# Optimization experiments

Measured on AMD Instinct MI355X. Metric: run time of the kernel, lower is better.

The kernel has to match this reference:

```python
import jax, jax.numpy as jnp
import numpy as np

N = 100000
E = 3200000
NODE_IN = 118
D = 32
H = 4
C = D // H  # 8
EDGE_DIM = 50 + 3
L = 4
LN_EPS = 1e-5


def _layernorm(x, g, b):
    mu = jnp.mean(x, axis=-1, keepdims=True)
    var = jnp.mean(jnp.square(x - mu), axis=-1, keepdims=True)
    return (x - mu) * jax.lax.rsqrt(var + LN_EPS) * g + b


def setup_inputs() -> dict:
    key = jax.random.key(0)
    ks = jax.random.split(key, 20)
    x = jax.random.normal(ks[0], (N, NODE_IN), dtype=jnp.float32)
    edge_index = jax.random.randint(ks[1], (2, E), 0, N, dtype=jnp.int32)
    edge_len = jax.random.normal(ks[2], (E, 50), dtype=jnp.float32)
    edge_vec = jax.random.normal(ks[3], (E, 3), dtype=jnp.float32)
    s_in = 1.0 / np.sqrt(NODE_IN)
    s_d = 1.0 / np.sqrt(D)
    s_e = 1.0 / np.sqrt(EDGE_DIM)
    node_in_W = jax.random.normal(ks[4], (NODE_IN, D), dtype=jnp.float32) * s_in
    node_in_b = jnp.zeros((D,), dtype=jnp.float32)
    ln_g = jnp.ones((L, D), dtype=jnp.float32)
    ln_b = jnp.zeros((L, D), dtype=jnp.float32)
    Wq = jax.random.normal(ks[5], (L, D, D), dtype=jnp.float32) * s_d
    bq = jnp.zeros((L, D), dtype=jnp.float32)
    Wk = jax.random.normal(ks[6], (L, D, D), dtype=jnp.float32) * s_d
    bk = jnp.zeros((L, D), dtype=jnp.float32)
    Wv = jax.random.normal(ks[7], (L, D, D), dtype=jnp.float32) * s_d
    bv = jnp.zeros((L, D), dtype=jnp.float32)
    We = jax.random.normal(ks[8], (L, EDGE_DIM, D), dtype=jnp.float32) * s_e  # lin_edge, bias=False
    Wskip = jax.random.normal(ks[9], (L, D, D), dtype=jnp.float32) * s_d
    bskip = jnp.zeros((L, D), dtype=jnp.float32)
    return {"x": x, "edge_index": edge_index, "edge_len": edge_len, "edge_vec": edge_vec,
            "node_in_W": node_in_W, "node_in_b": node_in_b, "ln_g": ln_g, "ln_b": ln_b,
            "Wq": Wq, "bq": bq, "Wk": Wk, "bk": bk, "Wv": Wv, "bv": bv,
            "We": We, "Wskip": Wskip, "bskip": bskip}


def reference(x, edge_index, edge_len, edge_vec, node_in_W, node_in_b, ln_g, ln_b,
              Wq, bq, Wk, bk, Wv, bv, We, Wskip, bskip):
    src = edge_index[0]  # j (source), messages flow source -> target
    dst = edge_index[1]  # i (target), softmax grouped by dst
    ef = jnp.concatenate([edge_len, edge_vec], axis=-1)  # [E, 53]
    h = x @ node_in_W + node_in_b  # [N, D]
    scale = 1.0 / np.sqrt(C)
    for l in range(L):
        xn = _layernorm(h, ln_g[l], ln_b[l])
        q = (xn @ Wq[l] + bq[l]).reshape(N, H, C)
        k = (xn @ Wk[l] + bk[l]).reshape(N, H, C)
        v = (xn @ Wv[l] + bv[l]).reshape(N, H, C)
        e = (ef @ We[l]).reshape(E, H, C)  # per-edge key/value shift
        kj = k[src] + e                     # [E, H, C]
        alpha = jnp.sum(q[dst] * kj, axis=-1) * scale  # [E, H]
        # segment softmax over incoming edges of each target node
        amax = jax.ops.segment_max(alpha, dst, num_segments=N)  # [N, H]
        amax = jnp.where(jnp.isfinite(amax), amax, 0.0)
        ex = jnp.exp(alpha - amax[dst])
        denom = jax.ops.segment_sum(ex, dst, num_segments=N)
        w = ex / (denom[dst] + 1e-16)       # [E, H]
        msg = (v[src] + e) * w[:, :, None]  # [E, H, C]
        agg = jax.ops.segment_sum(msg.reshape(E, H * C), dst, num_segments=N)  # [N, D]
        y = agg + xn @ Wskip[l] + bskip[l]  # concat heads + root skip (lin_skip(x_i))
        h = h + y                            # residual
    return h
```

## Files before the change

### kernel.cpp

```cpp
#include <hip/hip_runtime.h>
#include <hip/hip_bf16.h>
#include <math.h>

#define N_NODES 100000
#define N_EDGES 3200000
#define NODE_IN 118
#define DIM 32
#define EDF 53
#define NLAYER 4

typedef __attribute__((ext_vector_type(8))) short short8;
typedef __attribute__((ext_vector_type(4))) float f32x4;
typedef unsigned short u16;
typedef unsigned int u32;

static __device__ __forceinline__ float bfhi2f(u32 hi) {
    union { u32 i; float f; } x; x.i = hi; return x.f;
}
static __device__ __forceinline__ u16 f2bf(float f) {
    union { float f; u32 i; } x; x.f = f;
    u32 i = x.i;
    return (u16)((i + 0x7FFFu + ((i >> 16) & 1u)) >> 16);
}
static __device__ __forceinline__ u32 pk2bf(float a, float b) {
    u32 r;
    asm("v_cvt_pk_bf16_f32 %0, %1, %2" : "=v"(r) : "v"(a), "v"(b));
    return r;
}

__global__ __launch_bounds__(256) void k_count(const int* __restrict__ dst, int* __restrict__ cnt) {
    int e = blockIdx.x * 256 + threadIdx.x;
    atomicAdd(&cnt[dst[e]], 1);
}

__global__ __launch_bounds__(256) void k_scanA(const int* __restrict__ cnt, int* __restrict__ off,
                                               int* __restrict__ bsum) {
    __shared__ int s[256];
    int t = threadIdx.x; int i = blockIdx.x * 256 + t;
    int v = (i < N_NODES) ? cnt[i] : 0;
    s[t] = v; __syncthreads();
    for (int d = 1; d < 256; d <<= 1) {
        int x = (t >= d) ? s[t - d] : 0; __syncthreads();
        s[t] += x; __syncthreads();
    }
    if (i < N_NODES) off[i] = s[t] - v;
    if (t == 255) bsum[blockIdx.x] = s[t];
}

__global__ __launch_bounds__(512) void k_scanB(int* bsum, int nb) {
    __shared__ int s[512];
    int t = threadIdx.x;
    int v = (t < nb) ? bsum[t] : 0;
    s[t] = v; __syncthreads();
    for (int d = 1; d < 512; d <<= 1) {
        int x = (t >= d) ? s[t - d] : 0; __syncthreads();
        s[t] += x; __syncthreads();
    }
    if (t < nb) bsum[t] = s[t] - v;
}

__global__ __launch_bounds__(256) void k_scanC(int* off, const int* __restrict__ bsum) {
    int i = blockIdx.x * 256 + threadIdx.x;
    if (i < N_NODES) off[i] += bsum[blockIdx.x];
    if (i == 0) off[N_NODES] = N_EDGES;
}

__global__ __launch_bounds__(256) void k_fill(const int* __restrict__ src, const int* __restrict__ dst,
                                              const int* __restrict__ off, int* __restrict__ cur,
                                              int* __restrict__ eidx, int* __restrict__ esrc) {
    int e = blockIdx.x * 256 + threadIdx.x;
    int d = dst[e];
    int p = off[d] + atomicAdd(&cur[d], 1);
    eidx[p] = e;
    esrc[p] = src[e];
}

__global__ __launch_bounds__(256) void k_init(const float* __restrict__ x, const float* __restrict__ W,
                                              const float* __restrict__ b, float* __restrict__ h) {
    __shared__ float Ws[NODE_IN * DIM];
    __shared__ float xs[8][NODE_IN];
    int t = threadIdx.x;
    for (int i = t; i < NODE_IN * DIM; i += 256) Ws[i] = W[i];
    int nb = blockIdx.x * 8;
    for (int i = t; i < 8 * NODE_IN; i += 256) {
        int n = i / NODE_IN, j = i % NODE_IN;
        xs[n][j] = x[(size_t)(nb + n) * NODE_IN + j];
    }
    __syncthreads();
    int n = t >> 5, c = t & 31;
    float acc = b[c];
    #pragma unroll 2
    for (int j = 0; j < NODE_IN; j++) acc += xs[n][j] * Ws[j * DIM + c];
    h[(size_t)(nb + n) * DIM + c] = acc;
}

template <int NL>
__global__ __launch_bounds__(256) void k_egemm(const float* __restrict__ elen, const float* __restrict__ evec,
                                               const int* __restrict__ eidx, const float* __restrict__ We,
                                               u16* __restrict__ eout) {
    __shared__ u16 st[4][16 * 160];
    int tid = threadIdx.x;
    int lane = tid & 63;
    int wvl = tid >> 6;
    int wv = (blockIdx.x * 256 + tid) >> 6;
    int nw = (gridDim.x * 256) >> 6;
    int n15 = lane & 15, kb = lane >> 4;

    short8 bf[2][2 * NL];
    for (int s = 0; s < 2; s++) {
        for (int t = 0; t < 2 * NL; t++) {
            int n = t * 16 + n15;
            int lay = n >> 5, c = n & 31;
            short8 tmp;
            #pragma unroll
            for (int j = 0; j < 8; j++) {
                int kk = s * 32 + kb * 8 + j;
                float w = (kk < EDF) ? We[(size_t)lay * EDF * DIM + (size_t)kk * DIM + c] : 0.f;
                ((u16*)&tmp)[j] = f2bf(w);
            }
            bf[s][t] = tmp;
        }
    }

    const int NT = N_EDGES / 16;

    auto LOADD = [&](int eid, float* fv) {
        const float* lp = elen + (size_t)eid * 50;
        {
            const float2* p2 = (const float2*)(lp + kb * 8);
            #pragma unroll
            for (int j = 0; j < 4; j++) { float2 t2 = p2[j]; fv[2 * j] = t2.x; fv[2 * j + 1] = t2.y; }
        }
        if (kb < 2) {
            const float2* p2 = (const float2*)(lp + 32 + kb * 8);
            #pragma unroll
            for (int j = 0; j < 4; j++) { float2 t2 = p2[j]; fv[8 + 2 * j] = t2.x; fv[8 + 2 * j + 1] = t2.y; }
        } else if (kb == 2) {
            float2 t2 = *(const float2*)(lp + 48);
            const float* vp = evec + (size_t)eid * 3;
            fv[8] = t2.x; fv[9] = t2.y; fv[10] = vp[0]; fv[11] = vp[1]; fv[12] = vp[2];
            fv[13] = 0.f; fv[14] = 0.f; fv[15] = 0.f;
        } else {
            #pragma unroll
            for (int j = 8; j < 16; j++) fv[j] = 0.f;
        }
    };

    int eidA = (wv < NT) ? eidx[wv * 16 + n15] : 0;
    int t1 = wv + nw;
    int eidB = (t1 < NT) ? eidx[t1 * 16 + n15] : 0;
    float cur[16];
    if (wv < NT) LOADD(eidA, cur);

    for (int tile = wv; tile < NT; tile += nw) {
        int nxt = tile + nw;
        float nx[16];
        if (nxt < NT) LOADD(eidB, nx);
        int t2 = tile + 2 * nw;
        int eidC = (t2 < NT) ? eidx[t2 * 16 + n15] : 0;

        union { short8 s; u32 u[4]; } A0, A1;
        A0.u[0] = pk2bf(cur[0], cur[1]);   A0.u[1] = pk2bf(cur[2], cur[3]);
        A0.u[2] = pk2bf(cur[4], cur[5]);   A0.u[3] = pk2bf(cur[6], cur[7]);
        A1.u[0] = pk2bf(cur[8], cur[9]);   A1.u[1] = pk2bf(cur[10], cur[11]);
        A1.u[2] = pk2bf(cur[12], cur[13]); A1.u[3] = pk2bf(cur[14], cur[15]);

        u16* W = st[wvl];
        #pragma unroll
        for (int t = 0; t < 2 * NL; t++) {
            f32x4 z = {0.f, 0.f, 0.f, 0.f};
            z = __builtin_amdgcn_mfma_f32_16x16x32_bf16(A0.s, bf[0][t], z, 0, 0, 0);
            z = __builtin_amdgcn_mfma_f32_16x16x32_bf16(A1.s, bf[1][t], z, 0, 0, 0);
            int n = t * 16 + n15;
            #pragma unroll
            for (int r = 0; r < 4; r++) {
                int row = kb * 4 + r;
                int idx = row * 160 + (n ^ ((row & 12) << 2));
                W[idx] = f2bf(z[r]);
            }
        }
        int row = lane >> 2, q = lane & 3;
        size_t base2 = (size_t)(tile * 16) * (NL * 32);
        #pragma unroll
        for (int lay = 0; lay < NL; lay++) {
            int idx = row * 160 + ((lay * 32 + q * 8) ^ ((row & 12) << 2));
            short8 vblk = *(const short8*)&W[idx];
            *(short8*)&eout[base2 + (size_t)row * (NL * 32) + lay * 32 + q * 8] = vblk;
        }

        #pragma unroll
        for (int j = 0; j < 16; j++) cur[j] = nx[j];
        eidA = eidB; eidB = eidC;
    }
}

__global__ __launch_bounds__(256) void k_node(const float* __restrict__ h,
        const float* __restrict__ g, const float* __restrict__ bta,
        const float* __restrict__ Wq, const float* __restrict__ bq,
        const float* __restrict__ Wk, const float* __restrict__ bk,
        const float* __restrict__ Wv, const float* __restrict__ bv,
        const float* __restrict__ Ws, const float* __restrict__ bs,
        float* __restrict__ qo, u16* __restrict__ kvo, float* __restrict__ hso) {
    __shared__ float WQ[DIM * DIM], WK[DIM * DIM], WV[DIM * DIM], WS[DIM * DIM];
    __shared__ float xn[8][DIM];
    int t = threadIdx.x;
    for (int i = t; i < DIM * DIM; i += 256) { WQ[i] = Wq[i]; WK[i] = Wk[i]; WV[i] = Wv[i]; WS[i] = Ws[i]; }
    int n = t >> 5, c = t & 31;
    size_t node = (size_t)blockIdx.x * 8 + n;
    float hv = h[node * DIM + c];
    float s1 = hv;
    for (int d = 1; d < 32; d <<= 1) s1 += __shfl_xor(s1, d, 64);
    float mu = s1 * (1.f / 32.f);
    float dv = hv - mu;
    float s2 = dv * dv;
    for (int d = 1; d < 32; d <<= 1) s2 += __shfl_xor(s2, d, 64);
    float inv = rsqrtf(s2 * (1.f / 32.f) + 1e-5f);
    float xv = dv * inv * g[c] + bta[c];
    xn[n][c] = xv;
    __syncthreads();
    float aq = bq[c], ak = bk[c], av = bv[c], as = bs[c];
    #pragma unroll 4
    for (int j = 0; j < DIM; j++) {
        float xj = xn[n][j];
        aq += xj * WQ[j * DIM + c];
        ak += xj * WK[j * DIM + c];
        av += xj * WV[j * DIM + c];
        as += xj * WS[j * DIM + c];
    }
    size_t o = node * DIM + c;
    qo[o] = aq * 0.35355339059327373f;
    kvo[node * 64 + c]      = f2bf(ak);
    kvo[node * 64 + 32 + c] = f2bf(av);
    hso[o] = hv + as;
}

__global__ __launch_bounds__(256) void k_aggr(const int* __restrict__ off, const int* __restrict__ esrc,
        const u16* __restrict__ eb, int estr,
        const float* __restrict__ qb, const u16* __restrict__ kvb,
        const float* __restrict__ hs, float* __restrict__ out) {
    int tid = threadIdx.x;
    size_t node = (size_t)blockIdx.x * 4 + (tid >> 6);
    int lane = tid & 63;
    int eg = lane >> 2, hq = lane & 3, c0 = hq * 8;
    float4 q0 = *(const float4*)&qb[node * DIM + c0];
    float4 q1 = *(const float4*)&qb[node * DIM + c0 + 4];
    int o0 = off[node], o1 = off[node + 1];
    int safe = (o0 < N_EDGES) ? o0 : (N_EDGES - 1);
    float n0=0.f,n1=0.f,n2=0.f,n3=0.f,n4=0.f,n5=0.f,n6=0.f,n7=0.f;
    float dacc = 0.f;

    int pA = o0 + eg;  bool aA = pA < o1; int sA = esrc[aA ? pA : safe];
    int pB = pA + 16;  bool aB = pB < o1; int sB = esrc[aB ? pB : safe];
    int pC = pB + 16;  bool aC = pC < o1; int sC = esrc[aC ? pC : safe];
    int cA = aA ? pA : safe, cB = aB ? pB : safe, cCs = aC ? pC : safe;

    uint4 dAe = *(const uint4*)&eb[(size_t)cA * estr + c0];
    uint4 dAk = *(const uint4*)&kvb[(size_t)sA * 64 + c0];
    uint4 dAv = *(const uint4*)&kvb[(size_t)sA * 64 + 32 + c0];
    uint4 dBe = *(const uint4*)&eb[(size_t)cB * estr + c0];
    uint4 dBk = *(const uint4*)&kvb[(size_t)sB * 64 + c0];
    uint4 dBv = *(const uint4*)&kvb[(size_t)sB * 64 + 32 + c0];

    for (int p = o0; p < o1; p += 16) {
        uint4 dCe = *(const uint4*)&eb[(size_t)cCs * estr + c0];
        uint4 dCk = *(const uint4*)&kvb[(size_t)sC * 64 + c0];
        uint4 dCv = *(const uint4*)&kvb[(size_t)sC * 64 + 32 + c0];
        int pD = pC + 16; bool aD = pD < o1; int qD = aD ? pD : safe;
        int sD = esrc[qD];

        float e0 = bfhi2f(dAe.x << 16), e1 = bfhi2f(dAe.x & 0xFFFF0000u);
        float e2 = bfhi2f(dAe.y << 16), e3 = bfhi2f(dAe.y & 0xFFFF0000u);
        float e4 = bfhi2f(dAe.z << 16), e5 = bfhi2f(dAe.z & 0xFFFF0000u);
        float e6 = bfhi2f(dAe.w << 16), e7 = bfhi2f(dAe.w & 0xFFFF0000u);
        float k0 = bfhi2f(dAk.x << 16), k1 = bfhi2f(dAk.x & 0xFFFF0000u);
        float k2 = bfhi2f(dAk.y << 16), k3 = bfhi2f(dAk.y & 0xFFFF0000u);
        float k4 = bfhi2f(dAk.z << 16), k5 = bfhi2f(dAk.z & 0xFFFF0000u);
        float k6 = bfhi2f(dAk.w << 16), k7 = bfhi2f(dAk.w & 0xFFFF0000u);
        float v0 = bfhi2f(dAv.x << 16), v1 = bfhi2f(dAv.x & 0xFFFF0000u);
        float v2 = bfhi2f(dAv.y << 16), v3 = bfhi2f(dAv.y & 0xFFFF0000u);
        float v4 = bfhi2f(dAv.z << 16), v5 = bfhi2f(dAv.z & 0xFFFF0000u);
        float v6 = bfhi2f(dAv.w << 16), v7 = bfhi2f(dAv.w & 0xFFFF0000u);
        float a =      q0.x * (k0 + e0);
        a = fmaf(q0.y, k1 + e1, a);
        a = fmaf(q0.z, k2 + e2, a);
        a = fmaf(q0.w, k3 + e3, a);
        a = fmaf(q1.x, k4 + e4, a);
        a = fmaf(q1.y, k5 + e5, a);
        a = fmaf(q1.z, k6 + e6, a);
        a = fmaf(q1.w, k7 + e7, a);
        float ex = aA ? __expf(a) : 0.f;
        n0 = fmaf(ex, v0 + e0, n0); n1 = fmaf(ex, v1 + e1, n1);
        n2 = fmaf(ex, v2 + e2, n2); n3 = fmaf(ex, v3 + e3, n3);
        n4 = fmaf(ex, v4 + e4, n4); n5 = fmaf(ex, v5 + e5, n5);
        n6 = fmaf(ex, v6 + e6, n6); n7 = fmaf(ex, v7 + e7, n7);
        dacc += ex;

        aA = aB; dAe = dBe; dAk = dBk; dAv = dBv;
        dBe = dCe; dBk = dCk; dBv = dCv;
        aB = aC; aC = aD;
        cCs = qD; sC = sD; pC = pD;
    }
    #pragma unroll
    for (int d = 4; d < 64; d <<= 1) {
        n0 += __shfl_xor(n0, d); n1 += __shfl_xor(n1, d);
        n2 += __shfl_xor(n2, d); n3 += __shfl_xor(n3, d);
        n4 += __shfl_xor(n4, d); n5 += __shfl_xor(n5, d);
        n6 += __shfl_xor(n6, d); n7 += __shfl_xor(n7, d);
        dacc += __shfl_xor(dacc, d);
    }
    if (eg == 0) {
        float inv = 1.f / (dacc + 1e-16f);
        float4 h0 = *(const float4*)&hs[node * DIM + c0];
        float4 h1 = *(const float4*)&hs[node * DIM + c0 + 4];
        float4 o0v = { h0.x + n0 * inv, h0.y + n1 * inv, h0.z + n2 * inv, h0.w + n3 * inv };
        float4 o1v = { h1.x + n4 * inv, h1.y + n5 * inv, h1.z + n6 * inv, h1.w + n7 * inv };
        *(float4*)&out[node * DIM + c0] = o0v;
        *(float4*)&out[node * DIM + c0 + 4] = o1v;
    }
}

extern "C" void kernel_launch(void* const* d_in, const int* in_sizes, int n_in,
                              void* d_out, int out_size, void* d_ws, size_t ws_size,
                              hipStream_t stream) {
    const float* x    = (const float*)d_in[0];
    const int*   ei   = (const int*)d_in[1];
    const int*   src  = ei;
    const int*   dst  = ei + N_EDGES;
    const float* elen = (const float*)d_in[2];
    const float* evec = (const float*)d_in[3];
    const float* niW  = (const float*)d_in[4];
    const float* nib  = (const float*)d_in[5];
    const float* lng  = (const float*)d_in[6];
    const float* lnb  = (const float*)d_in[7];
    const float* Wq   = (const float*)d_in[8];
    const float* bq   = (const float*)d_in[9];
    const float* Wk   = (const float*)d_in[10];
    const float* bk   = (const float*)d_in[11];
    const float* Wv   = (const float*)d_in[12];
    const float* bv   = (const float*)d_in[13];
    const float* We   = (const float*)d_in[14];
    const float* Wsk  = (const float*)d_in[15];
    const float* bsk  = (const float*)d_in[16];
    float* out = (float*)d_out;

    unsigned char* w = (unsigned char*)d_ws;
    auto alloc = [&](size_t bytes) -> void* {
        void* p = (void*)w; w += (bytes + 255) & ~(size_t)255; return p;
    };
    int*   off  = (int*)alloc((N_NODES + 1) * sizeof(int));
    int*   cnt  = (int*)alloc(N_NODES * sizeof(int));
    int*   bsum = (int*)alloc(512 * sizeof(int));
    int*   eidx = (int*)alloc((size_t)N_EDGES * sizeof(int));
    int*   esrc = (int*)alloc((size_t)N_EDGES * sizeof(int));
    float* h    = (float*)alloc((size_t)N_NODES * DIM * sizeof(float));
    float* qb   = (float*)alloc((size_t)N_NODES * DIM * sizeof(float));
    u16*   kvb  = (u16*)alloc((size_t)N_NODES * 64 * sizeof(u16));
    float* hsb  = (float*)alloc((size_t)N_NODES * DIM * sizeof(float));
    size_t used = (size_t)(w - (unsigned char*)d_ws);
    size_t e_full = (size_t)NLAYER * N_EDGES * DIM * sizeof(u16);
    size_t e_one  = (size_t)N_EDGES * DIM * sizeof(u16);
    bool full = (used + e_full) <= ws_size;
    u16* ebuf = (u16*)alloc(full ? e_full : e_one);

    const int EB = N_EDGES / 256;
    const int NB = N_NODES / 8;
    const int AB = N_NODES / 4;
    const int nbScan = (N_NODES + 255) / 256;

    hipMemsetAsync(cnt, 0, N_NODES * sizeof(int), stream);
    k_count<<<EB, 256, 0, stream>>>(dst, cnt);
    k_scanA<<<nbScan, 256, 0, stream>>>(cnt, off, bsum);
    k_scanB<<<1, 512, 0, stream>>>(bsum, nbScan);
    k_scanC<<<nbScan, 256, 0, stream>>>(off, bsum);
    hipMemsetAsync(cnt, 0, N_NODES * sizeof(int), stream);
    k_fill<<<EB, 256, 0, stream>>>(src, dst, off, cnt, eidx, esrc);

    k_init<<<NB, 256, 0, stream>>>(x, niW, nib, h);

    if (full) k_egemm<4><<<4096, 256, 0, stream>>>(elen, evec, eidx, We, ebuf);

    for (int l = 0; l < NLAYER; l++) {
        if (!full) k_egemm<1><<<4096, 256, 0, stream>>>(elen, evec, eidx, We + (size_t)l * EDF * DIM, ebuf);
        k_node<<<NB, 256, 0, stream>>>(h, lng + l * DIM, lnb + l * DIM,
                                       Wq + (size_t)l * DIM * DIM, bq + l * DIM,
                                       Wk + (size_t)l * DIM * DIM, bk + l * DIM,
                                       Wv + (size_t)l * DIM * DIM, bv + l * DIM,
                                       Wsk + (size_t)l * DIM * DIM, bsk + l * DIM,
                                       qb, kvb, hsb);
        const u16* el = full ? (ebuf + (size_t)l * DIM) : ebuf;
        int estr = full ? (NLAYER * DIM) : DIM;
        k_aggr<<<AB, 256, 0, stream>>>(off, esrc, el, estr, qb, kvb, hsb,
                                       (l == NLAYER - 1) ? out : h);
    }
}
```

Before: 1.451 ms.

## Store edge features layer-major and pack four nodes per wave in aggregation

The precomputed per-edge projections are now written as separate contiguous per-layer planes instead of being interleaved across layers. Each edge row read in a layer is then a dense 64-byte block rather than a strided slice of a 256-byte row, which is meant to cut wasted memory traffic. The aggregation kernel now gives each wave four destination nodes, with four edge lanes per node instead of sixteen lanes on one node. This shortens the cross-lane reduction and launches fewer blocks. In exchange each node walks its edges in more loop iterations, and the loop count is set by the largest degree among the four nodes, which can cause divergence.

```diff
diff --git a/kernel.cpp b/kernel.cpp
--- a/kernel.cpp
+++ b/kernel.cpp
@@ -180,12 +180,11 @@
             }
         }
         int row = lane >> 2, q = lane & 3;
-        size_t base2 = (size_t)(tile * 16) * (NL * 32);
         #pragma unroll
         for (int lay = 0; lay < NL; lay++) {
             int idx = row * 160 + ((lay * 32 + q * 8) ^ ((row & 12) << 2));
             short8 vblk = *(const short8*)&W[idx];
-            *(short8*)&eout[base2 + (size_t)row * (NL * 32) + lay * 32 + q * 8] = vblk;
+            *(short8*)&eout[(size_t)lay * N_EDGES * DIM + ((size_t)tile * 16 + row) * DIM + q * 8] = vblk;
         }
 
         #pragma unroll
@@ -235,38 +234,41 @@
 }
 
 __global__ __launch_bounds__(256) void k_aggr(const int* __restrict__ off, const int* __restrict__ esrc,
-        const u16* __restrict__ eb, int estr,
+        const u16* __restrict__ eb,
         const float* __restrict__ qb, const u16* __restrict__ kvb,
         const float* __restrict__ hs, float* __restrict__ out) {
     int tid = threadIdx.x;
-    size_t node = (size_t)blockIdx.x * 4 + (tid >> 6);
     int lane = tid & 63;
-    int eg = lane >> 2, hq = lane & 3, c0 = hq * 8;
+    int ns = lane >> 4, eg = (lane >> 2) & 3, hq = lane & 3, c0 = hq * 8;
+    size_t node = (size_t)blockIdx.x * 16 + (size_t)(tid >> 6) * 4 + ns;
     float4 q0 = *(const float4*)&qb[node * DIM + c0];
     float4 q1 = *(const float4*)&qb[node * DIM + c0 + 4];
     int o0 = off[node], o1 = off[node + 1];
     int safe = (o0 < N_EDGES) ? o0 : (N_EDGES - 1);
+    int nit = (o1 - o0 + 3) >> 2;
+    nit = max(nit, __shfl_xor(nit, 16));
+    nit = max(nit, __shfl_xor(nit, 32));
+
     float n0=0.f,n1=0.f,n2=0.f,n3=0.f,n4=0.f,n5=0.f,n6=0.f,n7=0.f;
     float dacc = 0.f;
 
-    int pA = o0 + eg;  bool aA = pA < o1; int sA = esrc[aA ? pA : safe];
-    int pB = pA + 16;  bool aB = pB < o1; int sB = esrc[aB ? pB : safe];
-    int pC = pB + 16;  bool aC = pC < o1; int sC = esrc[aC ? pC : safe];
-    int cA = aA ? pA : safe, cB = aB ? pB : safe, cCs = aC ? pC : safe;
-
-    uint4 dAe = *(const uint4*)&eb[(size_t)cA * estr + c0];
+    int pA = o0 + eg;  bool aA = pA < o1; int cA = aA ? pA : safe; int sA = esrc[cA];
+    int pB = pA + 4;   bool aB = pB < o1; int cB = aB ? pB : safe; int sB = esrc[cB];
+    int pC = pB + 4;   bool aC = pC < o1; int cC = aC ? pC : safe; int sC = esrc[cC];
+
+    uint4 dAe = *(const uint4*)&eb[(size_t)cA * DIM + c0];
     uint4 dAk = *(const uint4*)&kvb[(size_t)sA * 64 + c0];
     uint4 dAv = *(const uint4*)&kvb[(size_t)sA * 64 + 32 + c0];
-    uint4 dBe = *(const uint4*)&eb[(size_t)cB * estr + c0];
+    uint4 dBe = *(const uint4*)&eb[(size_t)cB * DIM + c0];
     uint4 dBk = *(const uint4*)&kvb[(size_t)sB * 64 + c0];
     uint4 dBv = *(const uint4*)&kvb[(size_t)sB * 64 + 32 + c0];
 
-    for (int p = o0; p < o1; p += 16) {
-        uint4 dCe = *(const uint4*)&eb[(size_t)cCs * estr + c0];
+    for (int it = 0; it < nit; ++it) {
+        uint4 dCe = *(const uint4*)&eb[(size_t)cC * DIM + c0];
         uint4 dCk = *(const uint4*)&kvb[(size_t)sC * 64 + c0];
         uint4 dCv = *(const uint4*)&kvb[(size_t)sC * 64 + 32 + c0];
-        int pD = pC + 16; bool aD = pD < o1; int qD = aD ? pD : safe;
-        int sD = esrc[qD];
+        int pD = pC + 4; bool aD = pD < o1; int cD = aD ? pD : safe;
+        int sD = esrc[cD];
 
         float e0 = bfhi2f(dAe.x << 16), e1 = bfhi2f(dAe.x & 0xFFFF0000u);
         float e2 = bfhi2f(dAe.y << 16), e3 = bfhi2f(dAe.y & 0xFFFF0000u);
@@ -298,10 +300,10 @@
         aA = aB; dAe = dBe; dAk = dBk; dAv = dBv;
         dBe = dCe; dBk = dCk; dBv = dCv;
         aB = aC; aC = aD;
-        cCs = qD; sC = sD; pC = pD;
+        cC = cD; sC = sD; pC = pD;
     }
     #pragma unroll
-    for (int d = 4; d < 64; d <<= 1) {
+    for (int d = 4; d <= 8; d <<= 1) {
         n0 += __shfl_xor(n0, d); n1 += __shfl_xor(n1, d);
         n2 += __shfl_xor(n2, d); n3 += __shfl_xor(n3, d);
         n4 += __shfl_xor(n4, d); n5 += __shfl_xor(n5, d);
@@ -364,7 +366,7 @@
 
     const int EB = N_EDGES / 256;
     const int NB = N_NODES / 8;
-    const int AB = N_NODES / 4;
+    const int AB = N_NODES / 16;
     const int nbScan = (N_NODES + 255) / 256;
 
     hipMemsetAsync(cnt, 0, N_NODES * sizeof(int), stream);
@@ -387,9 +389,8 @@
                                        Wv + (size_t)l * DIM * DIM, bv + l * DIM,
                                        Wsk + (size_t)l * DIM * DIM, bsk + l * DIM,
                                        qb, kvb, hsb);
-        const u16* el = full ? (ebuf + (size_t)l * DIM) : ebuf;
-        int estr = full ? (NLAYER * DIM) : DIM;
-        k_aggr<<<AB, 256, 0, stream>>>(off, esrc, el, estr, qb, kvb, hsb,
+        const u16* el = full ? (ebuf + (size_t)l * N_EDGES * DIM) : ebuf;
+        k_aggr<<<AB, 256, 0, stream>>>(off, esrc, el, qb, kvb, hsb,
                                        (l == NLAYER - 1) ? out : h);
     }
 }
```

New measurement: 1.344 ms. -7.4%, faster.
